# Optimization experiments

Measured on AMD Instinct MI355X. Metric: run time of the kernel, lower is better.

Reference implementation:

```python
import jax, jax.numpy as jnp
import numpy as np

B, D, H = 131072, 8, 128


def setup_inputs() -> dict:
    key = jax.random.key(0)
    ks = jax.random.split(key, 8)
    s1 = 1.0 / np.sqrt(D + 1)
    s2 = 1.0 / np.sqrt(H)
    return {
        "z": jax.random.normal(ks[0], (B, D), dtype=jnp.float32),
        "logp_z": jnp.zeros((B, 1), dtype=jnp.float32),
        "t": jax.random.uniform(ks[1], (1,), dtype=jnp.float32),
        "W1": jax.random.normal(ks[2], (D + 1, H), dtype=jnp.float32) * s1,
        "b1": jnp.zeros((H,), dtype=jnp.float32),
        "W2": jax.random.normal(ks[3], (H, H), dtype=jnp.float32) * s2,
        "b2": jnp.zeros((H,), dtype=jnp.float32),
        "W3": jax.random.normal(ks[4], (H, D), dtype=jnp.float32) * s2,
        "b3": jnp.zeros((D,), dtype=jnp.float32),
    }


def _net_single(z_i, t_scalar, W1, b1, W2, b2, W3, b3):
    # z_i: [D] -> dz/dt: [D]; FFJORD-style MLP on concat([z, t])
    x = jnp.concatenate([z_i, t_scalar[None]])  # [D+1]
    h = jnp.tanh(x @ W1 + b1)
    h = jnp.tanh(h @ W2 + b2)
    return h @ W3 + b3


def reference(z, logp_z, t, W1, b1, W2, b2, W3, b3):
    t_scalar = t.reshape(())

    def f_i(z_i):
        return _net_single(z_i, t_scalar, W1, b1, W2, b2, W3, b3)

    # dz/dt for every sample (batched forward)
    dz_dt = jax.vmap(f_i)(z)  # [B, D]
    # Exact Jacobian trace: fused forward-mode batched Jacobian (replaces the
    # original's D sequential autograd.grad reverse-mode calls)
    jac = jax.vmap(jax.jacfwd(f_i))(z)  # [B, D, D]
    trace = jnp.einsum("bii->b", jac)  # [B]
    dlogp_z_dt = -trace[:, None]  # [B, 1]
    return (dz_dt, dlogp_z_dt)
```

## Files before the change

### kernel.cpp

```cpp
#include <hip/hip_runtime.h>
#include <hip/hip_bf16.h>

#define BATCH 131072
#define PITCH_H 72

typedef __bf16 bf16x4 __attribute__((ext_vector_type(4)));
typedef __bf16 bf16x8 __attribute__((ext_vector_type(8)));
typedef float floatx4 __attribute__((ext_vector_type(4)));

__device__ __forceinline__ float fast_tanh(float x) {
    float e = __expf(2.0f * x);
    return 1.0f - 2.0f * __builtin_amdgcn_rcpf(e + 1.0f);
}


__global__ void prep_kernel(const float* __restrict__ W1,
                            const float* __restrict__ W2,
                            const float* __restrict__ W3,
                            const float* __restrict__ b1,
                            __bf16* __restrict__ ws) {
    int idx = blockIdx.x * 256 + threadIdx.x;
    if (idx < 16384) {
        int j = idx & 7, q = (idx >> 3) & 3, n = (idx >> 5) & 127, kb = idx >> 12;
        int k = kb * 32 + q * 8 + j;
        ws[idx] = (__bf16)W2[k * 128 + n];
        float c = 0.0f;
        #pragma unroll
        for (int d = 0; d < 8; ++d) c += W3[k * 8 + d] * W1[d * 128 + n];
        ws[16384 + idx] = (__bf16)(W2[n * 128 + k] * c);
    } else if (idx < 20480) {
        int t = idx - 16384;
        int j = t & 7, q = (t >> 3) & 3, n = t >> 5;
        int k = q * 8 + j;
        __bf16 v = (__bf16)0.0f;
        if (k < 9) v = (__bf16)W1[k * 128 + n];
        else if (k == 9) v = (__bf16)b1[n];
        else if (k == 10) {
            float hi = (float)(__bf16)b1[n];
            v = (__bf16)(b1[n] - hi);
        }
        ws[32768 + t] = v;
    } else if (idx < 22528) {
        int t = idx - 20480;
        int j = t & 7, q = (t >> 3) & 3, n = (t >> 5) & 15, kb = t >> 9;
        int k = kb * 32 + q * 8 + j;
        ws[36864 + t] = (n < 8) ? (__bf16)W3[k * 8 + n] : (__bf16)0.0f;
    }
}

__global__ __launch_bounds__(256, 2) void cnf_main(
        const float* __restrict__ z, const float* __restrict__ t_ptr,
        const float* __restrict__ b1g, const float* __restrict__ b2g,
        const float* __restrict__ b3g, const __bf16* __restrict__ ws,
        float* __restrict__ out) {
    __shared__ __bf16 sW2s[16384];
    __shared__ __bf16 sGTs[16384];
    __shared__ float sb2f[128];
    __shared__ __align__(16) __bf16 tile[4][16 * PITCH_H];

    const int tid = threadIdx.x;
    const int lane = tid & 63;
    const int w = tid >> 6;
    const int p = lane & 15;
    const int q = lane >> 4;
    const int sbase = blockIdx.x * 128 + w * 32;
    const float tval = t_ptr[0];

    bf16x8 ax0, ax1;
    #pragma unroll
    for (int j = 0; j < 8; ++j) { ax0[j] = (__bf16)0.0f; ax1[j] = (__bf16)0.0f; }
    if (q == 0) {
        const float4* zp0 = (const float4*)(z + (size_t)(sbase + p) * 8);
        const float4* zp1 = (const float4*)(z + (size_t)(sbase + 16 + p) * 8);
        const float4 a0 = zp0[0], a1 = zp0[1], c0 = zp1[0], c1 = zp1[1];
        ax0[0] = (__bf16)a0.x; ax0[1] = (__bf16)a0.y;
        ax0[2] = (__bf16)a0.z; ax0[3] = (__bf16)a0.w;
        ax0[4] = (__bf16)a1.x; ax0[5] = (__bf16)a1.y;
        ax0[6] = (__bf16)a1.z; ax0[7] = (__bf16)a1.w;
        ax1[0] = (__bf16)c0.x; ax1[1] = (__bf16)c0.y;
        ax1[2] = (__bf16)c0.z; ax1[3] = (__bf16)c0.w;
        ax1[4] = (__bf16)c1.x; ax1[5] = (__bf16)c1.y;
        ax1[6] = (__bf16)c1.z; ax1[7] = (__bf16)c1.w;
    } else if (q == 1) {
        ax0[0] = (__bf16)tval; ax0[1] = (__bf16)1.0f; ax0[2] = (__bf16)1.0f;
        ax1[0] = (__bf16)tval; ax1[1] = (__bf16)1.0f; ax1[2] = (__bf16)1.0f;
    }

    const bf16x8* W1g = (const bf16x8*)(ws + 32768);
    const bf16x8* W3g = (const bf16x8*)(ws + 36864);
    bf16x8 w1f[8];
    #pragma unroll
    for (int nt = 0; nt < 8; ++nt) w1f[nt] = W1g[(nt * 16 + p) * 4 + q];
    bf16x8 w3f[4];
    #pragma unroll
    for (int kb = 0; kb < 4; ++kb) w3f[kb] = W3g[(kb * 16 + p) * 4 + q];
    floatx4 b3f = {0.f, 0.f, 0.f, 0.f};
    if (q < 2) b3f = *(const floatx4*)(b3g + q * 4);

    {
        uint4* dst = (uint4*)sW2s;
        const uint4* src = (const uint4*)ws;
        #pragma unroll
        for (int i = 0; i < 8; ++i) dst[tid + i * 256] = src[tid + i * 256];
        uint4* dstg = (uint4*)sGTs;
        const uint4* srcg = (const uint4*)(ws + 16384);
        #pragma unroll
        for (int i = 0; i < 8; ++i) dstg[tid + i * 256] = srcg[tid + i * 256];
        if (tid < 128) sb2f[tid] = b2g[tid];
    }

    __bf16* T = tile[w];

    float a1c0[32], a1c1[32];
    bf16x8 aha[4], ahb[4];
    #pragma unroll
    for (int h = 0; h < 2; ++h) {
        floatx4 accA[4], accB[4];
        #pragma unroll
        for (int lt = 0; lt < 4; ++lt) {
            const floatx4 zz = {0.f, 0.f, 0.f, 0.f};
            accA[lt] = __builtin_amdgcn_mfma_f32_16x16x32_bf16(w1f[4 * h + lt], ax0, zz, 0, 0, 0);
            accB[lt] = __builtin_amdgcn_mfma_f32_16x16x32_bf16(w1f[4 * h + lt], ax1, zz, 0, 0, 0);
        }
        #pragma unroll
        for (int lt = 0; lt < 4; ++lt) {
            bf16x4 v;
            #pragma unroll
            for (int r = 0; r < 4; ++r) {
                const float h1 = fast_tanh(accA[lt][r]);
                a1c0[(4 * h + lt) * 4 + r] = __builtin_fmaf(-h1, h1, 1.0f);
                v[r] = (__bf16)h1;
            }
            *(bf16x4*)&T[p * PITCH_H + lt * 16 + q * 4] = v;
        }
        aha[2 * h]     = *(const bf16x8*)&T[p * PITCH_H + q * 8];
        aha[2 * h + 1] = *(const bf16x8*)&T[p * PITCH_H + 32 + q * 8];
        #pragma unroll
        for (int lt = 0; lt < 4; ++lt) {
            bf16x4 v;
            #pragma unroll
            for (int r = 0; r < 4; ++r) {
                const float h1 = fast_tanh(accB[lt][r]);
                a1c1[(4 * h + lt) * 4 + r] = __builtin_fmaf(-h1, h1, 1.0f);
                v[r] = (__bf16)h1;
            }
            *(bf16x4*)&T[p * PITCH_H + lt * 16 + q * 4] = v;
        }
        ahb[2 * h]     = *(const bf16x8*)&T[p * PITCH_H + q * 8];
        ahb[2 * h + 1] = *(const bf16x8*)&T[p * PITCH_H + 32 + q * 8];
    }

    __syncthreads();
    const bf16x8* W2sv = (const bf16x8*)sW2s;
    const bf16x8* GTsv = (const bf16x8*)sGTs;

    bf16x8 ah2a[4], ah2b[4];
    #pragma unroll
    for (int h = 0; h < 2; ++h) {
        floatx4 accA[4], accB[4];
        #pragma unroll
        for (int lt = 0; lt < 4; ++lt) {
            const int nt = 4 * h + lt;
            const floatx4 binit = *(const floatx4*)&sb2f[nt * 16 + q * 4];
            floatx4 a = binit, b = binit;
            #pragma unroll
            for (int kb = 0; kb < 4; ++kb) {
                const bf16x8 wf = W2sv[(kb * 128 + nt * 16 + p) * 4 + q];
                a = __builtin_amdgcn_mfma_f32_16x16x32_bf16(wf, aha[kb], a, 0, 0, 0);
                b = __builtin_amdgcn_mfma_f32_16x16x32_bf16(wf, ahb[kb], b, 0, 0, 0);
            }
            accA[lt] = a; accB[lt] = b;
        }
        #pragma unroll
        for (int lt = 0; lt < 4; ++lt) {
            bf16x4 v;
            #pragma unroll
            for (int r = 0; r < 4; ++r) v[r] = (__bf16)fast_tanh(accA[lt][r]);
            *(bf16x4*)&T[p * PITCH_H + lt * 16 + q * 4] = v;
        }
        ah2a[2 * h]     = *(const bf16x8*)&T[p * PITCH_H + q * 8];
        ah2a[2 * h + 1] = *(const bf16x8*)&T[p * PITCH_H + 32 + q * 8];
        #pragma unroll
        for (int lt = 0; lt < 4; ++lt) {
            bf16x4 v;
            #pragma unroll
            for (int r = 0; r < 4; ++r) v[r] = (__bf16)fast_tanh(accB[lt][r]);
            *(bf16x4*)&T[p * PITCH_H + lt * 16 + q * 4] = v;
        }
        ah2b[2 * h]     = *(const bf16x8*)&T[p * PITCH_H + q * 8];
        ah2b[2 * h + 1] = *(const bf16x8*)&T[p * PITCH_H + 32 + q * 8];
    }

    floatx4 d3A = b3f, d3B = b3f;
    #pragma unroll
    for (int kb = 0; kb < 4; ++kb) {
        d3A = __builtin_amdgcn_mfma_f32_16x16x32_bf16(w3f[kb], ah2a[kb], d3A, 0, 0, 0);
        d3B = __builtin_amdgcn_mfma_f32_16x16x32_bf16(w3f[kb], ah2b[kb], d3B, 0, 0, 0);
    }
    if (q < 2) {
        *(floatx4*)(out + (size_t)(sbase + p) * 8 + q * 4) = d3A;
        *(floatx4*)(out + (size_t)(sbase + 16 + p) * 8 + q * 4) = d3B;
    }

    bf16x8 aaA[4], aaB[4];
    #pragma unroll
    for (int kb = 0; kb < 4; ++kb) {
        #pragma unroll
        for (int j = 0; j < 8; ++j) {
            const float fa = (float)ah2a[kb][j];
            aaA[kb][j] = (__bf16)__builtin_fmaf(-fa, fa, 1.0f);
            const float fb = (float)ah2b[kb][j];
            aaB[kb][j] = (__bf16)__builtin_fmaf(-fb, fb, 1.0f);
        }
    }

    float trA = 0.f, trB = 0.f;
    #pragma unroll
    for (int nt = 0; nt < 8; ++nt) {
        floatx4 uA = {0.f, 0.f, 0.f, 0.f}, uB = {0.f, 0.f, 0.f, 0.f};
        #pragma unroll
        for (int kb = 0; kb < 4; ++kb) {
            const bf16x8 gf = GTsv[(kb * 128 + nt * 16 + p) * 4 + q];
            uA = __builtin_amdgcn_mfma_f32_16x16x32_bf16(gf, aaA[kb], uA, 0, 0, 0);
            uB = __builtin_amdgcn_mfma_f32_16x16x32_bf16(gf, aaB[kb], uB, 0, 0, 0);
        }
        #pragma unroll
        for (int r = 0; r < 4; ++r) {
            trA = __builtin_fmaf(a1c0[nt * 4 + r], uA[r], trA);
            trB = __builtin_fmaf(a1c1[nt * 4 + r], uB[r], trB);
        }
    }
    trA += __shfl_xor(trA, 16, 64);
    trA += __shfl_xor(trA, 32, 64);
    trB += __shfl_xor(trB, 16, 64);
    trB += __shfl_xor(trB, 32, 64);
    if (lane < 16) {
        out[(size_t)BATCH * 8 + sbase + p] = -trA;
        out[(size_t)BATCH * 8 + sbase + 16 + p] = -trB;
    }
}

extern "C" void kernel_launch(void* const* d_in, const int* in_sizes, int n_in,
                              void* d_out, int out_size, void* d_ws, size_t ws_size,
                              hipStream_t stream) {
    const float* z  = (const float*)d_in[0];
    const float* t  = (const float*)d_in[2];
    const float* W1 = (const float*)d_in[3];
    const float* b1 = (const float*)d_in[4];
    const float* W2 = (const float*)d_in[5];
    const float* b2 = (const float*)d_in[6];
    const float* W3 = (const float*)d_in[7];
    const float* b3 = (const float*)d_in[8];
    __bf16* ws = (__bf16*)d_ws;
    float* out = (float*)d_out;

    prep_kernel<<<88, 256, 0, stream>>>(W1, W2, W3, b1, ws);
    cnf_main<<<1024, 256, 0, stream>>>(z, t, b1, b2, b3, ws, out);
}
```

Measured before the change: 89.95 us.

## Use async global-to-LDS weight loads and process two sample tiles per block

Weight staging into shared memory now uses global_load_lds direct transfers instead of register round-trips, overlapping with layer-1 compute. Each block handles two 128-sample tiles (grid halved) so the W2/GT LDS fill is amortized across twice the work, with the next tile's z prefetched during the first iteration. This trades fewer blocks (512 on 256 CUs, occupancy 2) and more register pressure for reduced per-block setup cost.

New measurement: 88.06 us, median of 2. 2.1% less time.

```diff
diff --git a/kernel.cpp b/kernel.cpp
--- a/kernel.cpp
+++ b/kernel.cpp
@@ -7,6 +7,9 @@
 typedef __bf16 bf16x4 __attribute__((ext_vector_type(4)));
 typedef __bf16 bf16x8 __attribute__((ext_vector_type(8)));
 typedef float floatx4 __attribute__((ext_vector_type(4)));
+
+#define GLOBAL_AS __attribute__((address_space(1)))
+#define LDS_AS __attribute__((address_space(3)))
 
 __device__ __forceinline__ float fast_tanh(float x) {
     float e = __expf(2.0f * x);
@@ -63,28 +66,7 @@
     const int w = tid >> 6;
     const int p = lane & 15;
     const int q = lane >> 4;
-    const int sbase = blockIdx.x * 128 + w * 32;
     const float tval = t_ptr[0];
-
-    bf16x8 ax0, ax1;
-    #pragma unroll
-    for (int j = 0; j < 8; ++j) { ax0[j] = (__bf16)0.0f; ax1[j] = (__bf16)0.0f; }
-    if (q == 0) {
-        const float4* zp0 = (const float4*)(z + (size_t)(sbase + p) * 8);
-        const float4* zp1 = (const float4*)(z + (size_t)(sbase + 16 + p) * 8);
-        const float4 a0 = zp0[0], a1 = zp0[1], c0 = zp1[0], c1 = zp1[1];
-        ax0[0] = (__bf16)a0.x; ax0[1] = (__bf16)a0.y;
-        ax0[2] = (__bf16)a0.z; ax0[3] = (__bf16)a0.w;
-        ax0[4] = (__bf16)a1.x; ax0[5] = (__bf16)a1.y;
-        ax0[6] = (__bf16)a1.z; ax0[7] = (__bf16)a1.w;
-        ax1[0] = (__bf16)c0.x; ax1[1] = (__bf16)c0.y;
-        ax1[2] = (__bf16)c0.z; ax1[3] = (__bf16)c0.w;
-        ax1[4] = (__bf16)c1.x; ax1[5] = (__bf16)c1.y;
-        ax1[6] = (__bf16)c1.z; ax1[7] = (__bf16)c1.w;
-    } else if (q == 1) {
-        ax0[0] = (__bf16)tval; ax0[1] = (__bf16)1.0f; ax0[2] = (__bf16)1.0f;
-        ax1[0] = (__bf16)tval; ax1[1] = (__bf16)1.0f; ax1[2] = (__bf16)1.0f;
-    }
 
     const bf16x8* W1g = (const bf16x8*)(ws + 32768);
     const bf16x8* W3g = (const bf16x8*)(ws + 36864);
@@ -96,147 +78,199 @@
     for (int kb = 0; kb < 4; ++kb) w3f[kb] = W3g[(kb * 16 + p) * 4 + q];
     floatx4 b3f = {0.f, 0.f, 0.f, 0.f};
     if (q < 2) b3f = *(const floatx4*)(b3g + q * 4);
-
+    const float b2v = (tid < 128) ? b2g[tid] : 0.0f;
+
+    float4 zc0a, zc1a, zc0b, zc1b;
     {
-        uint4* dst = (uint4*)sW2s;
-        const uint4* src = (const uint4*)ws;
-        #pragma unroll
-        for (int i = 0; i < 8; ++i) dst[tid + i * 256] = src[tid + i * 256];
-        uint4* dstg = (uint4*)sGTs;
-        const uint4* srcg = (const uint4*)(ws + 16384);
-        #pragma unroll
-        for (int i = 0; i < 8; ++i) dstg[tid + i * 256] = srcg[tid + i * 256];
-        if (tid < 128) sb2f[tid] = b2g[tid];
+        const int sb0 = blockIdx.x * 256 + w * 32;
+        if (q == 0) {
+            const float4* zp0 = (const float4*)(z + (size_t)(sb0 + p) * 8);
+            const float4* zp1 = (const float4*)(z + (size_t)(sb0 + 16 + p) * 8);
+            zc0a = zp0[0]; zc1a = zp0[1]; zc0b = zp1[0]; zc1b = zp1[1];
+        }
+    }
+
+    {
+        const uint4* srcW2v = (const uint4*)ws;
+        const uint4* srcGTv = (const uint4*)(ws + 16384);
+        uint4* dstW2v = (uint4*)sW2s;
+        uint4* dstGTv = (uint4*)sGTs;
+        #pragma unroll
+        for (int i = 0; i < 8; ++i) {
+            const int idx = tid + i * 256;
+            const int wbase = w * 64 + i * 256;
+            __builtin_amdgcn_global_load_lds(
+                (const GLOBAL_AS uint4*)(srcW2v + idx),
+                (LDS_AS uint4*)(dstW2v + wbase), 16, 0, 0);
+            __builtin_amdgcn_global_load_lds(
+                (const GLOBAL_AS uint4*)(srcGTv + idx),
+                (LDS_AS uint4*)(dstGTv + wbase), 16, 0, 0);
+        }
     }
 
     __bf16* T = tile[w];
-
-    float a1c0[32], a1c1[32];
-    bf16x8 aha[4], ahb[4];
-    #pragma unroll
-    for (int h = 0; h < 2; ++h) {
-        floatx4 accA[4], accB[4];
-        #pragma unroll
-        for (int lt = 0; lt < 4; ++lt) {
-            const floatx4 zz = {0.f, 0.f, 0.f, 0.f};
-            accA[lt] = __builtin_amdgcn_mfma_f32_16x16x32_bf16(w1f[4 * h + lt], ax0, zz, 0, 0, 0);
-            accB[lt] = __builtin_amdgcn_mfma_f32_16x16x32_bf16(w1f[4 * h + lt], ax1, zz, 0, 0, 0);
-        }
-        #pragma unroll
-        for (int lt = 0; lt < 4; ++lt) {
-            bf16x4 v;
-            #pragma unroll
-            for (int r = 0; r < 4; ++r) {
-                const float h1 = fast_tanh(accA[lt][r]);
-                a1c0[(4 * h + lt) * 4 + r] = __builtin_fmaf(-h1, h1, 1.0f);
-                v[r] = (__bf16)h1;
-            }
-            *(bf16x4*)&T[p * PITCH_H + lt * 16 + q * 4] = v;
-        }
-        aha[2 * h]     = *(const bf16x8*)&T[p * PITCH_H + q * 8];
-        aha[2 * h + 1] = *(const bf16x8*)&T[p * PITCH_H + 32 + q * 8];
-        #pragma unroll
-        for (int lt = 0; lt < 4; ++lt) {
-            bf16x4 v;
-            #pragma unroll
-            for (int r = 0; r < 4; ++r) {
-                const float h1 = fast_tanh(accB[lt][r]);
-                a1c1[(4 * h + lt) * 4 + r] = __builtin_fmaf(-h1, h1, 1.0f);
-                v[r] = (__bf16)h1;
-            }
-            *(bf16x4*)&T[p * PITCH_H + lt * 16 + q * 4] = v;
-        }
-        ahb[2 * h]     = *(const bf16x8*)&T[p * PITCH_H + q * 8];
-        ahb[2 * h + 1] = *(const bf16x8*)&T[p * PITCH_H + 32 + q * 8];
-    }
-
-    __syncthreads();
     const bf16x8* W2sv = (const bf16x8*)sW2s;
     const bf16x8* GTsv = (const bf16x8*)sGTs;
 
-    bf16x8 ah2a[4], ah2b[4];
+    float4 zn0a, zn1a, zn0b, zn1b;
+
     #pragma unroll
-    for (int h = 0; h < 2; ++h) {
-        floatx4 accA[4], accB[4];
-        #pragma unroll
-        for (int lt = 0; lt < 4; ++lt) {
-            const int nt = 4 * h + lt;
-            const floatx4 binit = *(const floatx4*)&sb2f[nt * 16 + q * 4];
-            floatx4 a = binit, b = binit;
+    for (int it = 0; it < 2; ++it) {
+        const int sbase = blockIdx.x * 256 + it * 128 + w * 32;
+
+        bf16x8 ax0, ax1;
+        #pragma unroll
+        for (int j = 0; j < 8; ++j) { ax0[j] = (__bf16)0.0f; ax1[j] = (__bf16)0.0f; }
+        if (q == 0) {
+            ax0[0] = (__bf16)zc0a.x; ax0[1] = (__bf16)zc0a.y;
+            ax0[2] = (__bf16)zc0a.z; ax0[3] = (__bf16)zc0a.w;
+            ax0[4] = (__bf16)zc1a.x; ax0[5] = (__bf16)zc1a.y;
+            ax0[6] = (__bf16)zc1a.z; ax0[7] = (__bf16)zc1a.w;
+            ax1[0] = (__bf16)zc0b.x; ax1[1] = (__bf16)zc0b.y;
+            ax1[2] = (__bf16)zc0b.z; ax1[3] = (__bf16)zc0b.w;
+            ax1[4] = (__bf16)zc1b.x; ax1[5] = (__bf16)zc1b.y;
+            ax1[6] = (__bf16)zc1b.z; ax1[7] = (__bf16)zc1b.w;
+        } else if (q == 1) {
+            ax0[0] = (__bf16)tval; ax0[1] = (__bf16)1.0f; ax0[2] = (__bf16)1.0f;
+            ax1[0] = (__bf16)tval; ax1[1] = (__bf16)1.0f; ax1[2] = (__bf16)1.0f;
+        }
+
+        float a1c0[32], a1c1[32];
+        bf16x8 aha[4], ahb[4];
+        #pragma unroll
+        for (int h = 0; h < 2; ++h) {
+            floatx4 accA[4], accB[4];
+            #pragma unroll
+            for (int lt = 0; lt < 4; ++lt) {
+                const floatx4 zz = {0.f, 0.f, 0.f, 0.f};
+                accA[lt] = __builtin_amdgcn_mfma_f32_16x16x32_bf16(w1f[4 * h + lt], ax0, zz, 0, 0, 0);
+                accB[lt] = __builtin_amdgcn_mfma_f32_16x16x32_bf16(w1f[4 * h + lt], ax1, zz, 0, 0, 0);
+            }
+            #pragma unroll
+            for (int lt = 0; lt < 4; ++lt) {
+                bf16x4 v;
+                #pragma unroll
+                for (int r = 0; r < 4; ++r) {
+                    const float h1 = fast_tanh(accA[lt][r]);
+                    a1c0[(4 * h + lt) * 4 + r] = __builtin_fmaf(-h1, h1, 1.0f);
+                    v[r] = (__bf16)h1;
+                }
+                *(bf16x4*)&T[p * PITCH_H + lt * 16 + q * 4] = v;
+            }
+            aha[2 * h]     = *(const bf16x8*)&T[p * PITCH_H + q * 8];
+            aha[2 * h + 1] = *(const bf16x8*)&T[p * PITCH_H + 32 + q * 8];
+            #pragma unroll
+            for (int lt = 0; lt < 4; ++lt) {
+                bf16x4 v;
+                #pragma unroll
+                for (int r = 0; r < 4; ++r) {
+                    const float h1 = fast_tanh(accB[lt][r]);
+                    a1c1[(4 * h + lt) * 4 + r] = __builtin_fmaf(-h1, h1, 1.0f);
+                    v[r] = (__bf16)h1;
+                }
+                *(bf16x4*)&T[p * PITCH_H + lt * 16 + q * 4] = v;
+            }
+            ahb[2 * h]     = *(const bf16x8*)&T[p * PITCH_H + q * 8];
+            ahb[2 * h + 1] = *(const bf16x8*)&T[p * PITCH_H + 32 + q * 8];
+        }
+
+        if (it == 0) {
+            if (q == 0) {
+                const int sb1i = blockIdx.x * 256 + 128 + w * 32;
+                const float4* zp0 = (const float4*)(z + (size_t)(sb1i + p) * 8);
+                const float4* zp1 = (const float4*)(z + (size_t)(sb1i + 16 + p) * 8);
+                zn0a = zp0[0]; zn1a = zp0[1]; zn0b = zp1[0]; zn1b = zp1[1];
+            }
+            if (tid < 128) sb2f[tid] = b2v;
+            __syncthreads();
+        }
+
+        bf16x8 ah2a[4], ah2b[4];
+        #pragma unroll
+        for (int h = 0; h < 2; ++h) {
+            floatx4 accA[4], accB[4];
+            #pragma unroll
+            for (int lt = 0; lt < 4; ++lt) {
+                const int nt = 4 * h + lt;
+                const floatx4 binit = *(const floatx4*)&sb2f[nt * 16 + q * 4];
+                floatx4 a = binit, b = binit;
+                #pragma unroll
+                for (int kb = 0; kb < 4; ++kb) {
+                    const bf16x8 wf = W2sv[(kb * 128 + nt * 16 + p) * 4 + q];
+                    a = __builtin_amdgcn_mfma_f32_16x16x32_bf16(wf, aha[kb], a, 0, 0, 0);
+                    b = __builtin_amdgcn_mfma_f32_16x16x32_bf16(wf, ahb[kb], b, 0, 0, 0);
+                }
+                accA[lt] = a; accB[lt] = b;
+            }
+            #pragma unroll
+            for (int lt = 0; lt < 4; ++lt) {
+                bf16x4 v;
+                #pragma unroll
+                for (int r = 0; r < 4; ++r) v[r] = (__bf16)fast_tanh(accA[lt][r]);
+                *(bf16x4*)&T[p * PITCH_H + lt * 16 + q * 4] = v;
+            }
+            ah2a[2 * h]     = *(const bf16x8*)&T[p * PITCH_H + q * 8];
+            ah2a[2 * h + 1] = *(const bf16x8*)&T[p * PITCH_H + 32 + q * 8];
+            #pragma unroll
+            for (int lt = 0; lt < 4; ++lt) {
+                bf16x4 v;
+                #pragma unroll
+                for (int r = 0; r < 4; ++r) v[r] = (__bf16)fast_tanh(accB[lt][r]);
+                *(bf16x4*)&T[p * PITCH_H + lt * 16 + q * 4] = v;
+            }
+            ah2b[2 * h]     = *(const bf16x8*)&T[p * PITCH_H + q * 8];
+            ah2b[2 * h + 1] = *(const bf16x8*)&T[p * PITCH_H + 32 + q * 8];
+        }
+
+        floatx4 d3A = b3f, d3B = b3f;
+        #pragma unroll
+        for (int kb = 0; kb < 4; ++kb) {
+            d3A = __builtin_amdgcn_mfma_f32_16x16x32_bf16(w3f[kb], ah2a[kb], d3A, 0, 0, 0);
+            d3B = __builtin_amdgcn_mfma_f32_16x16x32_bf16(w3f[kb], ah2b[kb], d3B, 0, 0, 0);
+        }
+        if (q < 2) {
+            *(floatx4*)(out + (size_t)(sbase + p) * 8 + q * 4) = d3A;
+            *(floatx4*)(out + (size_t)(sbase + 16 + p) * 8 + q * 4) = d3B;
+        }
+
+        bf16x8 aaA[4], aaB[4];
+        #pragma unroll
+        for (int kb = 0; kb < 4; ++kb) {
+            #pragma unroll
+            for (int j = 0; j < 8; ++j) {
+                const float fa = (float)ah2a[kb][j];
+                aaA[kb][j] = (__bf16)__builtin_fmaf(-fa, fa, 1.0f);
+                const float fb = (float)ah2b[kb][j];
+                aaB[kb][j] = (__bf16)__builtin_fmaf(-fb, fb, 1.0f);
+            }
+        }
+
+        float trA = 0.f, trB = 0.f;
+        #pragma unroll
+        for (int nt = 0; nt < 8; ++nt) {
+            floatx4 uA = {0.f, 0.f, 0.f, 0.f}, uB = {0.f, 0.f, 0.f, 0.f};
             #pragma unroll
             for (int kb = 0; kb < 4; ++kb) {
-                const bf16x8 wf = W2sv[(kb * 128 + nt * 16 + p) * 4 + q];
-                a = __builtin_amdgcn_mfma_f32_16x16x32_bf16(wf, aha[kb], a, 0, 0, 0);
-                b = __builtin_amdgcn_mfma_f32_16x16x32_bf16(wf, ahb[kb], b, 0, 0, 0);
-            }
-            accA[lt] = a; accB[lt] = b;
-        }
-        #pragma unroll
-        for (int lt = 0; lt < 4; ++lt) {
-            bf16x4 v;
-            #pragma unroll
-            for (int r = 0; r < 4; ++r) v[r] = (__bf16)fast_tanh(accA[lt][r]);
-            *(bf16x4*)&T[p * PITCH_H + lt * 16 + q * 4] = v;
-        }
-        ah2a[2 * h]     = *(const bf16x8*)&T[p * PITCH_H + q * 8];
-        ah2a[2 * h + 1] = *(const bf16x8*)&T[p * PITCH_H + 32 + q * 8];
-        #pragma unroll
-        for (int lt = 0; lt < 4; ++lt) {
-            bf16x4 v;
-            #pragma unroll
-            for (int r = 0; r < 4; ++r) v[r] = (__bf16)fast_tanh(accB[lt][r]);
-            *(bf16x4*)&T[p * PITCH_H + lt * 16 + q * 4] = v;
-        }
-        ah2b[2 * h]     = *(const bf16x8*)&T[p * PITCH_H + q * 8];
-        ah2b[2 * h + 1] = *(const bf16x8*)&T[p * PITCH_H + 32 + q * 8];
-    }
-
-    floatx4 d3A = b3f, d3B = b3f;
-    #pragma unroll
-    for (int kb = 0; kb < 4; ++kb) {
-        d3A = __builtin_amdgcn_mfma_f32_16x16x32_bf16(w3f[kb], ah2a[kb], d3A, 0, 0, 0);
-        d3B = __builtin_amdgcn_mfma_f32_16x16x32_bf16(w3f[kb], ah2b[kb], d3B, 0, 0, 0);
-    }
-    if (q < 2) {
-        *(floatx4*)(out + (size_t)(sbase + p) * 8 + q * 4) = d3A;
-        *(floatx4*)(out + (size_t)(sbase + 16 + p) * 8 + q * 4) = d3B;
-    }
-
-    bf16x8 aaA[4], aaB[4];
-    #pragma unroll
-    for (int kb = 0; kb < 4; ++kb) {
-        #pragma unroll
-        for (int j = 0; j < 8; ++j) {
-            const float fa = (float)ah2a[kb][j];
-            aaA[kb][j] = (__bf16)__builtin_fmaf(-fa, fa, 1.0f);
-            const float fb = (float)ah2b[kb][j];
-            aaB[kb][j] = (__bf16)__builtin_fmaf(-fb, fb, 1.0f);
-        }
-    }
-
-    float trA = 0.f, trB = 0.f;
-    #pragma unroll
-    for (int nt = 0; nt < 8; ++nt) {
-        floatx4 uA = {0.f, 0.f, 0.f, 0.f}, uB = {0.f, 0.f, 0.f, 0.f};
-        #pragma unroll
-        for (int kb = 0; kb < 4; ++kb) {
-            const bf16x8 gf = GTsv[(kb * 128 + nt * 16 + p) * 4 + q];
-            uA = __builtin_amdgcn_mfma_f32_16x16x32_bf16(gf, aaA[kb], uA, 0, 0, 0);
-            uB = __builtin_amdgcn_mfma_f32_16x16x32_bf16(gf, aaB[kb], uB, 0, 0, 0);
-        }
-        #pragma unroll
-        for (int r = 0; r < 4; ++r) {
-            trA = __builtin_fmaf(a1c0[nt * 4 + r], uA[r], trA);
-            trB = __builtin_fmaf(a1c1[nt * 4 + r], uB[r], trB);
-        }
-    }
-    trA += __shfl_xor(trA, 16, 64);
-    trA += __shfl_xor(trA, 32, 64);
-    trB += __shfl_xor(trB, 16, 64);
-    trB += __shfl_xor(trB, 32, 64);
-    if (lane < 16) {
-        out[(size_t)BATCH * 8 + sbase + p] = -trA;
-        out[(size_t)BATCH * 8 + sbase + 16 + p] = -trB;
+                const bf16x8 gf = GTsv[(kb * 128 + nt * 16 + p) * 4 + q];
+                uA = __builtin_amdgcn_mfma_f32_16x16x32_bf16(gf, aaA[kb], uA, 0, 0, 0);
+                uB = __builtin_amdgcn_mfma_f32_16x16x32_bf16(gf, aaB[kb], uB, 0, 0, 0);
+            }
+            #pragma unroll
+            for (int r = 0; r < 4; ++r) {
+                trA = __builtin_fmaf(a1c0[nt * 4 + r], uA[r], trA);
+                trB = __builtin_fmaf(a1c1[nt * 4 + r], uB[r], trB);
+            }
+        }
+        trA += __shfl_xor(trA, 16, 64);
+        trA += __shfl_xor(trA, 32, 64);
+        trB += __shfl_xor(trB, 16, 64);
+        trB += __shfl_xor(trB, 32, 64);
+        if (lane < 16) {
+            out[(size_t)BATCH * 8 + sbase + p] = -trA;
+            out[(size_t)BATCH * 8 + sbase + 16 + p] = -trB;
+        }
+
+        if (it == 0) { zc0a = zn0a; zc1a = zn1a; zc0b = zn0b; zc1b = zn1b; }
     }
 }
 
@@ -255,5 +289,5 @@
     float* out = (float*)d_out;
 
     prep_kernel<<<88, 256, 0, stream>>>(W1, W2, W3, b1, ws);
-    cnf_main<<<1024, 256, 0, stream>>>(z, t, b1, b2, b3, ws, out);
-}
+    cnf_main<<<512, 256, 0, stream>>>(z, t, b1, b2, b3, ws, out);
+}
```
